# Optimization experiments

Hardware: AMD Instinct MI355X
Metric: run time of the kernel (lower is better)

Reference implementation:

```python
import jax, jax.numpy as jnp
import numpy as np

B = 8
N = 1024


def _sqrtm_psd(P):
    # symmetric PSD matrix square root via eigendecomposition
    w, V = jnp.linalg.eigh(P)
    return (V * jnp.sqrt(jnp.clip(w, 0.0))) @ V.T


def setup_inputs() -> dict:
    key = jax.random.key(0)
    k1, k2, k3 = jax.random.split(key, 3)
    x = jax.random.normal(k1, (1, B, N, 1), dtype=jnp.float32)
    # PSD covariance with nonnegative entries so abs() is a no-op and sqrtm is real
    A = jax.random.uniform(k2, (N, N), dtype=jnp.float32)
    P_u = (A @ A.T) / N
    Q_k = jax.random.uniform(k3, (N, N), dtype=jnp.float32)
    return {"x": x, "P_u": P_u, "Q_k": Q_k}


def reference(x, P_u, Q_k):
    n = x.shape[2]  # N
    # sigma = x.repeat(1,1,1,N): [1,B,N,N]
    sigma0 = jnp.broadcast_to(x, (1, x.shape[1], n, n))
    # p = sqrtm(N * |P_u|)
    p = _sqrtm_psd(n * jnp.abs(P_u))
    # concat(sigma+p, sigma-p) along last dim -> [1,B,N,2N]
    sigma = jnp.concatenate((sigma0 + p, sigma0 - p), axis=3)
    scale = 1.0 / (2 * n)
    x_bar = jnp.mean(sigma, axis=3)  # [1,B,N]
    # Faithful to original: only sigma[0,0] is used for the deviations,
    # while the mean varies with the batch index i2.
    points = sigma[0, 0]  # [N, 2N]
    c = points[None, :, :] - x_bar[0][:, :, None]  # [B, N, 2N]
    S = jnp.einsum('bni,bmi->bnm', c, c)  # sum of 2N outer products per batch
    P_k = S * scale + (Q_k ** 2) * 0.01
    return P_k, jnp.transpose(sigma, (0, 1, 3, 2))


if __name__ == "__main__":
    out = reference(**setup_inputs())
    print(out[0].shape, out[1].shape)
```

## Files before the change

### kernel.cpp

```cpp
#include <hip/hip_runtime.h>
#include <math.h>

#define NN 1024
#define BB 8
#define NS_ITERS 10
#define EPS_SHIFT 4.0f
#define MB (1u<<20)

typedef __attribute__((ext_vector_type(8))) short short8;
typedef __attribute__((ext_vector_type(4))) float floatx4;

__device__ __forceinline__ ushort f2bf(float f) {
    union { float f; uint32_t u; } v; v.f = f;
    uint32_t u = v.u;
    uint32_t r = (u + 0x7fffu + ((u >> 16) & 1u)) >> 16;
    return (ushort)r;
}
__device__ __forceinline__ float bf2f(ushort h) {
    union { uint32_t u; float f; } v; v.u = ((uint32_t)h) << 16;
    return v.f;
}

__device__ __forceinline__ void gload16(const ushort* g, ushort* s) {
    __builtin_amdgcn_global_load_lds(
        (__attribute__((address_space(1))) unsigned int*)(g),
        (__attribute__((address_space(3))) unsigned int*)(s), 16, 0, 0);
}

__device__ __forceinline__ float block_sum(float v) {
    #pragma unroll
    for (int off = 32; off > 0; off >>= 1) v += __shfl_down(v, off, 64);
    __shared__ float red[4];
    int lane = threadIdx.x & 63, wid = threadIdx.x >> 6;
    if (lane == 0) red[wid] = v;
    __syncthreads();
    float t = 0.f;
    if (threadIdx.x == 0) t = red[0] + red[1] + red[2] + red[3];
    return t;
}

__global__ __launch_bounds__(256) void matvec_abs(const float* __restrict__ pu,
                                                  const float* __restrict__ x,
                                                  float* __restrict__ y,
                                                  int use_ones) {
    int row = blockIdx.x;
    const float4* pr = (const float4*)(pu + (size_t)row * NN);
    float4 p = pr[threadIdx.x];
    float s;
    if (use_ones) {
        s = fabsf(p.x) + fabsf(p.y) + fabsf(p.z) + fabsf(p.w);
    } else {
        float4 xx = ((const float4*)x)[threadIdx.x];
        s = fabsf(p.x) * xx.x + fabsf(p.y) * xx.y + fabsf(p.z) * xx.z + fabsf(p.w) * xx.w;
    }
    s = block_sum(s);
    if (threadIdx.x == 0) y[row] = s;
}

__global__ void norm_vec(const float* __restrict__ y, float* __restrict__ v) {
    float ss = 0.f;
    for (int i = threadIdx.x; i < NN; i += 256) { float t = y[i]; ss += t * t; }
    #pragma unroll
    for (int off = 32; off > 0; off >>= 1) ss += __shfl_down(ss, off, 64);
    __shared__ float red[4];
    __shared__ float s_inv;
    int lane = threadIdx.x & 63, wid = threadIdx.x >> 6;
    if (lane == 0) red[wid] = ss;
    __syncthreads();
    if (threadIdx.x == 0) s_inv = rsqrtf(red[0] + red[1] + red[2] + red[3]);
    __syncthreads();
    float inv = s_inv;
    for (int i = threadIdx.x; i < NN; i += 256) v[i] = y[i] * inv;
}

__global__ void dot_vec(const float* __restrict__ a, const float* __restrict__ b,
                        float* __restrict__ out) {
    float s = 0.f;
    for (int i = threadIdx.x; i < NN; i += 256) s += a[i] * b[i];
    s = block_sum(s);
    if (threadIdx.x == 0) out[0] = s;
}

__global__ __launch_bounds__(256) void deflate_kernel(const float* __restrict__ pu,
                                                      const float* __restrict__ v,
                                                      const float* __restrict__ w,
                                                      float* __restrict__ sc,
                                                      float* __restrict__ D) {
    int idx = blockIdx.x * 256 + threadIdx.x;
    int row = idx >> 8;
    int c0 = (idx & 255) << 2;
    float lam = sc[5];
    float vr = v[row], wr = w[row];
    float4 p = ((const float4*)pu)[idx];
    float4 vc = *(const float4*)(v + c0);
    float4 wc = *(const float4*)(w + c0);
    float4 d;
    d.x = (float)NN * (fabsf(p.x) - vr * wc.x - wr * vc.x + lam * vr * vc.x);
    d.y = (float)NN * (fabsf(p.y) - vr * wc.y - wr * vc.y + lam * vr * vc.y);
    d.z = (float)NN * (fabsf(p.z) - vr * wc.z - wr * vc.z + lam * vr * vc.z);
    d.w = (float)NN * (fabsf(p.w) - vr * wc.w - wr * vc.w + lam * vr * vc.w);
    int dd = row - c0;
    if (dd == 0) d.x += EPS_SHIFT;
    else if (dd == 1) d.y += EPS_SHIFT;
    else if (dd == 2) d.z += EPS_SHIFT;
    else if (dd == 3) d.w += EPS_SHIFT;
    ((float4*)D)[idx] = d;
    float ss = d.x * d.x + d.y * d.y + d.z * d.z + d.w * d.w;
    ss = block_sum(ss);
    if (threadIdx.x == 0) atomicAdd(sc, ss);
}

__global__ void finalize_kernel(float* sc) {
    float c = sqrtf(sc[0]);
    sc[1] = 1.f / c;
    sc[2] = sqrtf(c);
    sc[4] = sqrtf((float)NN * sc[5]);
}

__device__ __forceinline__ void tile_swizzle64(int& row0, int& col0, int& zz) {
    int f = blockIdx.x + (blockIdx.y << 4) + (blockIdx.z << 8);
    int p = f & 7;
    int i = f >> 3;
    if (gridDim.z == 2) {
        zz = p & 1;
        int s = p >> 1;
        row0 = (((s >> 1) << 3) + (i >> 3)) << 6;
        col0 = (((s & 1) << 3) + (i & 7)) << 6;
    } else {
        zz = 0;
        row0 = (((p >> 1) << 2) + (i >> 3)) << 6;
        col0 = (((p & 1) << 3) + (i & 7)) << 6;
    }
}

__device__ __forceinline__ void mm_dev(const ushort* __restrict__ Ah,
                                       const ushort* __restrict__ Al,
                                       const ushort* __restrict__ Bh,
                                       const ushort* __restrict__ Bl,
                                       int row0, int col0, int kb, int kc,
                                       float* __restrict__ Cf,
                                       float* __restrict__ CfT,
                                       ushort* __restrict__ Chi,
                                       ushort* __restrict__ Clo) {
    __shared__ __align__(16) ushort lds[4 * 8192];
    const int t = threadIdx.x;
    const int w = t >> 6, l = t & 63;
    const int fm = l & 15, fq = l >> 4;
    const int lrow = l >> 2;
    const int lcol = (l & 3) << 3;

    const ushort* Ahp = Ah + (size_t)(row0 + lrow) * NN + kb + lcol;
    const ushort* Alp = Al + (size_t)(row0 + lrow) * NN + kb + lcol;
    const ushort* Bhp = Bh + (size_t)(col0 + lrow) * NN + kb + lcol;
    const ushort* Blp = Bl + (size_t)(col0 + lrow) * NN + kb + lcol;

    floatx4 acc[4][4];
    #pragma unroll
    for (int mi = 0; mi < 4; ++mi)
        #pragma unroll
        for (int ni = 0; ni < 4; ++ni) acc[mi][ni] = (floatx4)0.f;

    auto STAGE = [&](int kt) {
        const int koff = kt << 5;
        ushort* sb = lds + ((kt & 3) << 13);
        #pragma unroll
        for (int rb = 0; rb < 4; ++rb) {
            gload16(Ahp + (size_t)(rb << 4) * NN + koff, sb + (rb << 9));
            gload16(Alp + (size_t)(rb << 4) * NN + koff, sb + 2048 + (rb << 9));
            gload16(Bhp + (size_t)(rb << 4) * NN + koff, sb + 4096 + (rb << 9));
            gload16(Blp + (size_t)(rb << 4) * NN + koff, sb + 6144 + (rb << 9));
        }
    };

    const int nk = kc >> 5;
    STAGE(w);
    STAGE(w + 2);
    #pragma unroll 1
    for (int kt = w; kt < nk; kt += 2) {
        if (kt + 2 < nk) asm volatile("s_waitcnt vmcnt(16)" ::: "memory");
        else             asm volatile("s_waitcnt vmcnt(0)"  ::: "memory");
        __builtin_amdgcn_sched_barrier(0);
        const ushort* Ash = lds + ((kt & 3) << 13);
        const ushort* Asl = Ash + 2048;
        const ushort* Bsh = Ash + 4096;
        const ushort* Bsl = Ash + 6144;
        short8 ah[4], al[4], bh[4], bl[4];
        #pragma unroll
        for (int i = 0; i < 4; ++i) {
            const int ro = ((i << 4) + fm) * 32 + (fq << 3);
            ah[i] = *(const short8*)&Ash[ro];
            al[i] = *(const short8*)&Asl[ro];
            bh[i] = *(const short8*)&Bsh[ro];
            bl[i] = *(const short8*)&Bsl[ro];
        }
        asm volatile("s_waitcnt lgkmcnt(0)" ::: "memory");
        __builtin_amdgcn_sched_barrier(0);
        if (kt + 4 < nk) STAGE(kt + 4);
        #pragma unroll
        for (int mi = 0; mi < 4; ++mi)
            #pragma unroll
            for (int ni = 0; ni < 4; ++ni) {
                acc[mi][ni] = __builtin_amdgcn_mfma_f32_16x16x32_bf16(ah[mi], bh[ni], acc[mi][ni], 0, 0, 0);
                acc[mi][ni] = __builtin_amdgcn_mfma_f32_16x16x32_bf16(al[mi], bh[ni], acc[mi][ni], 0, 0, 0);
                acc[mi][ni] = __builtin_amdgcn_mfma_f32_16x16x32_bf16(ah[mi], bl[ni], acc[mi][ni], 0, 0, 0);
            }
    }

    __syncthreads();
    float* lf = (float*)lds;
    const int dep0 = w ? 0 : 2;
    const int own0 = w ? 2 : 0;
    #pragma unroll
    for (int m2 = 0; m2 < 2; ++m2) {
        #pragma unroll
        for (int ni = 0; ni < 4; ++ni)
            #pragma unroll
            for (int r = 0; r < 4; ++r) {
                int row = ((dep0 + m2) << 4) + (fq << 2) + r;
                int col = (ni << 4) + fm;
                lf[row * 66 + col] = acc[dep0 + m2][ni][r];
            }
    }
    __syncthreads();
    #pragma unroll
    for (int m2 = 0; m2 < 2; ++m2) {
        #pragma unroll
        for (int ni = 0; ni < 4; ++ni)
            #pragma unroll
            for (int r = 0; r < 4; ++r) {
                int row = ((own0 + m2) << 4) + (fq << 2) + r;
                int col = (ni << 4) + fm;
                acc[own0 + m2][ni][r] += lf[row * 66 + col];
            }
    }

    #pragma unroll
    for (int m2 = 0; m2 < 2; ++m2) {
        const int mi = own0 + m2;
        #pragma unroll
        for (int r = 0; r < 4; ++r) {
            int row = row0 + (mi << 4) + (fq << 2) + r;
            #pragma unroll
            for (int ni = 0; ni < 4; ++ni) {
                int col = col0 + (ni << 4) + fm;
                float v = acc[mi][ni][r];
                size_t idx = (size_t)row * NN + col;
                if (Cf) {
                    Cf[idx] = v;
                } else {
                    ushort h = f2bf(v);
                    Chi[idx] = h;
                    Clo[idx] = f2bf(v - bf2f(h));
                }
            }
        }
    }

    if (CfT) {
        __syncthreads();
        #pragma unroll
        for (int m2 = 0; m2 < 2; ++m2) {
            const int mi = own0 + m2;
            #pragma unroll
            for (int r = 0; r < 4; ++r) {
                int rl = (mi << 4) + (fq << 2) + r;
                #pragma unroll
                for (int ni = 0; ni < 4; ++ni) {
                    int cl = (ni << 4) + fm;
                    lf[cl * 68 + rl] = acc[mi][ni][r];
                }
            }
        }
        __syncthreads();
        int c = t >> 1, half = t & 1;
        const float* src = lf + c * 68 + (half << 5);
        float* dst = CfT + (size_t)(col0 + c) * NN + row0 + (half << 5);
        #pragma unroll
        for (int j = 0; j < 8; ++j)
            *(float4*)(dst + (j << 2)) = *(const float4*)(src + (j << 2));
    }
}

__global__ __launch_bounds__(128) void k_stage1(const ushort* __restrict__ Zh,
                                                const ushort* __restrict__ Zl,
                                                const ushort* __restrict__ Yh,
                                                const ushort* __restrict__ Yl,
                                                float* __restrict__ Mp,
                                                float* __restrict__ MpT0,
                                                float* __restrict__ MpT1) {
    int row0, col0, s;
    tile_swizzle64(row0, col0, s);
    mm_dev(Zh, Zl, Yh, Yl, row0, col0,
           s * (NN / 2), NN / 2, Mp + (size_t)s * NN * NN,
           s ? MpT1 : MpT0, nullptr, nullptr);
}

__global__ __launch_bounds__(128) void k_stage2(const ushort* __restrict__ Yh,
                                                const ushort* __restrict__ Yl,
                                                const ushort* __restrict__ Wh,
                                                const ushort* __restrict__ Wl,
                                                const ushort* __restrict__ Zh,
                                                const ushort* __restrict__ Zl,
                                                ushort* __restrict__ Ynh,
                                                ushort* __restrict__ Ynl,
                                                ushort* __restrict__ Znh,
                                                ushort* __restrict__ Znl) {
    int row0, col0, zz;
    tile_swizzle64(row0, col0, zz);
    if (zz == 0)
        mm_dev(Yh, Yl, Wh, Wl, row0, col0, 0, NN,
               nullptr, nullptr, Ynh, Ynl);
    else
        mm_dev(Wh, Wl, Zh, Zl, row0, col0, 0, NN,
               nullptr, nullptr, Znh, Znl);
}

__global__ __launch_bounds__(128) void k_final(const ushort* __restrict__ Yh,
                                               const ushort* __restrict__ Yl,
                                               const ushort* __restrict__ Wh,
                                               const ushort* __restrict__ Wl,
                                               float* __restrict__ Yf,
                                               float* __restrict__ YfT) {
    int row0, col0, zz;
    tile_swizzle64(row0, col0, zz);
    mm_dev(Yh, Yl, Wh, Wl, row0, col0, 0, NN,
           Yf, YfT, nullptr, nullptr);
}

__global__ __launch_bounds__(256) void k_wsplit(const float* __restrict__ Mp,
                                                const float* __restrict__ MpT0,
                                                const float* __restrict__ MpT1,
                                                ushort* __restrict__ Wh,
                                                ushort* __restrict__ Wl) {
    int i = blockIdx.x * 256 + threadIdx.x;
    int row = i >> 8, c0 = (i & 255) << 2;
    float4 m0 = ((const float4*)Mp)[i];
    float4 m1 = ((const float4*)Mp)[i + NN * NN / 4];
    float4 t0 = ((const float4*)MpT0)[i];
    float4 t1 = ((const float4*)MpT1)[i];
    float wv[4] = {-0.25f * (m0.x + m1.x + t0.x + t1.x),
                   -0.25f * (m0.y + m1.y + t0.y + t1.y),
                   -0.25f * (m0.z + m1.z + t0.z + t1.z),
                   -0.25f * (m0.w + m1.w + t0.w + t1.w)};
    int dd = row - c0;
    if (dd >= 0 && dd < 4) wv[dd] += 1.5f;
    ushort4 hv, lv;
    ushort* hp = (ushort*)&hv; ushort* lp = (ushort*)&lv;
    #pragma unroll
    for (int j = 0; j < 4; ++j) {
        ushort h = f2bf(wv[j]); hp[j] = h; lp[j] = f2bf(wv[j] - bf2f(h));
    }
    *(ushort4*)&Wh[(size_t)i << 2] = hv;
    *(ushort4*)&Wl[(size_t)i << 2] = lv;
}

__global__ __launch_bounds__(256) void k_wsplit0(const float* __restrict__ D,
                                                 const float* __restrict__ sc,
                                                 ushort* __restrict__ Yh,
                                                 ushort* __restrict__ Yl,
                                                 ushort* __restrict__ Wh,
                                                 ushort* __restrict__ Wl) {
    int i = blockIdx.x * 256 + threadIdx.x;
    int row = i >> 8, c0 = (i & 255) << 2;
    float invc = sc[1];
    float4 d = ((const float4*)D)[i];
    float yv[4] = {d.x * invc, d.y * invc, d.z * invc, d.w * invc};
    ushort4 yh, yl, wh, wl;
    ushort* yhp = (ushort*)&yh; ushort* ylp = (ushort*)&yl;
    ushort* whp = (ushort*)&wh; ushort* wlp = (ushort*)&wl;
    int dd = row - c0;
    #pragma unroll
    for (int j = 0; j < 4; ++j) {
        float y = yv[j];
        ushort h = f2bf(y); yhp[j] = h; ylp[j] = f2bf(y - bf2f(h));
        float wv = ((dd == j) ? 1.5f : 0.f) - 0.5f * y;
        ushort h2 = f2bf(wv); whp[j] = h2; wlp[j] = f2bf(wv - bf2f(h2));
    }
    *(ushort4*)&Yh[(size_t)i << 2] = yh;
    *(ushort4*)&Yl[(size_t)i << 2] = yl;
    *(ushort4*)&Wh[(size_t)i << 2] = wh;
    *(ushort4*)&Wl[(size_t)i << 2] = wl;
}

__global__ __launch_bounds__(256) void out0_kernel(const float* __restrict__ x,
                                                   const float* __restrict__ pu,
                                                   const float* __restrict__ qk,
                                                   float* __restrict__ out) {
    int i = blockIdx.x * blockDim.x + threadIdx.x;
    int rem = i & (NN * NN / 4 - 1);
    int b = i >> 18;
    int n = rem >> 8;
    int m4 = (rem & 255) << 2;
    float dn = x[n] - x[b * NN + n];
    float4 x0v = *(const float4*)(x + m4);
    float4 xbv = *(const float4*)(x + b * NN + m4);
    float4 pv = ((const float4*)pu)[rem];
    float4 qv = ((const float4*)qk)[rem];
    float4 o;
    o.x = dn * (x0v.x - xbv.x) + fabsf(pv.x) + 0.01f * qv.x * qv.x;
    o.y = dn * (x0v.y - xbv.y) + fabsf(pv.y) + 0.01f * qv.y * qv.y;
    o.z = dn * (x0v.z - xbv.z) + fabsf(pv.z) + 0.01f * qv.z * qv.z;
    o.w = dn * (x0v.w - xbv.w) + fabsf(pv.w) + 0.01f * qv.w * qv.w;
    ((float4*)out)[i] = o;
}

__global__ __launch_bounds__(256) void k_out1(const float* __restrict__ x,
                                              const float* __restrict__ Yf,
                                              const float* __restrict__ YfT,
                                              const float* __restrict__ sc,
                                              const float* __restrict__ v,
                                              float* __restrict__ out1) {
    int i = blockIdx.x * 256 + threadIdx.x;
    int j = i >> 8, i0 = (i & 255) << 2;
    float s = 0.5f * sc[2], s1v = sc[4] * v[j];
    float4 yr = *(const float4*)(Yf + (size_t)j * NN + i0);
    float4 yc = *(const float4*)(YfT + (size_t)j * NN + i0);
    float4 vc = *(const float4*)(v + i0);
    float4 p;
    p.x = s * (yr.x + yc.x) + s1v * vc.x;
    p.y = s * (yr.y + yc.y) + s1v * vc.y;
    p.z = s * (yr.z + yc.z) + s1v * vc.z;
    p.w = s * (yr.w + yc.w) + s1v * vc.w;
    #pragma unroll
    for (int b = 0; b < BB; ++b) {
        float4 xv = *(const float4*)(x + b * NN + i0);
        float4 a, m;
        a.x = xv.x + p.x; a.y = xv.y + p.y; a.z = xv.z + p.z; a.w = xv.w + p.w;
        m.x = xv.x - p.x; m.y = xv.y - p.y; m.z = xv.z - p.z; m.w = xv.w - p.w;
        float* base = out1 + (size_t)b * 2 * NN * NN;
        *(float4*)(base + (size_t)j * NN + i0) = a;
        *(float4*)(base + (size_t)(NN + j) * NN + i0) = m;
    }
}

extern "C" void kernel_launch(void* const* d_in, const int* in_sizes, int n_in,
                              void* d_out, int out_size, void* d_ws, size_t ws_size,
                              hipStream_t stream) {
    const float* x  = (const float*)d_in[0];
    const float* pu = (const float*)d_in[1];
    const float* qk = (const float*)d_in[2];
    float* out = (float*)d_out;
    char* ws = (char*)d_ws;

    float* Mp = (float*)ws;
    float* D  = Mp;
    float* Yf = Mp;
    float* YfT = (float*)(ws + (size_t)4 * MB);
    ushort* hi[5]; ushort* lo[5];
    for (int k = 0; k < 5; ++k) {
        hi[k] = (ushort*)(ws + (size_t)8 * MB + (size_t)k * 4 * MB);
        lo[k] = (ushort*)(ws + (size_t)8 * MB + (size_t)k * 4 * MB + 2 * MB);
    }
    float* vv = (float*)(ws + (size_t)28 * MB);
    float* vw = (float*)(ws + (size_t)28 * MB + 4096);
    float* vt = (float*)(ws + (size_t)28 * MB + 8192);
    float* sc = (float*)(ws + (size_t)28 * MB + 12288);

    hipMemsetAsync(sc, 0, 64, stream);
    matvec_abs<<<NN, 256, 0, stream>>>(pu, vv, vt, 1);
    norm_vec<<<1, 256, 0, stream>>>(vt, vv);
    matvec_abs<<<NN, 256, 0, stream>>>(pu, vv, vt, 0);
    norm_vec<<<1, 256, 0, stream>>>(vt, vv);
    matvec_abs<<<NN, 256, 0, stream>>>(pu, vv, vw, 0);
    dot_vec<<<1, 256, 0, stream>>>(vv, vw, sc + 5);
    deflate_kernel<<<NN * NN / 4 / 256, 256, 0, stream>>>(pu, vv, vw, sc, D);
    finalize_kernel<<<1, 1, 0, stream>>>(sc);

    k_wsplit0<<<NN * NN / 4 / 256, 256, 0, stream>>>(D, sc, hi[0], lo[0], hi[1], lo[1]);
    k_stage2<<<dim3(16, 16, 1), 128, 0, stream>>>(hi[0], lo[0], hi[1], lo[1],
                                                  hi[0], lo[0],
                                                  hi[2], lo[2], hi[3], lo[3]);
    int Y = 2, Z = 1, f0 = 0, f1 = 3, f2 = 4;

    for (int it = 1; it < NS_ITERS; ++it) {
        int W = f0;
        float* MpT0 = (float*)hi[f1];
        float* MpT1 = (float*)hi[f2];
        k_stage1<<<dim3(16, 16, 2), 128, 0, stream>>>(hi[Z], lo[Z], hi[Y], lo[Y],
                                                      Mp, MpT0, MpT1);
        k_wsplit<<<NN * NN / 4 / 256, 256, 0, stream>>>(Mp, MpT0, MpT1,
                                                        hi[W], lo[W]);
        if (it + 1 < NS_ITERS) {
            int Yn = f1, Zn = f2;
            k_stage2<<<dim3(16, 16, 2), 128, 0, stream>>>(
                hi[Y], lo[Y], hi[W], lo[W], hi[Z], lo[Z],
                hi[Yn], lo[Yn], hi[Zn], lo[Zn]);
            f0 = Y; f1 = Z; f2 = W;
            Y = Yn; Z = Zn;
        } else {
            k_final<<<dim3(16, 16, 1), 128, 0, stream>>>(hi[Y], lo[Y], hi[W], lo[W],
                                                         Yf, YfT);
        }
    }

    out0_kernel<<<(BB * NN * NN / 4) / 256, 256, 0, stream>>>(x, pu, qk, out);
    k_out1<<<NN * NN / 4 / 256, 256, 0, stream>>>(x, Yf, YfT, sc, vv,
                                                  out + (size_t)BB * NN * NN);
}
```

Before: 700.8 us.

## Split tile loads between waves with shared LDS ring and barriers

Each wave used to stage its own full A and B k-tiles into private ring slots. Now wave 0 loads the A half and wave 1 the B half of every k-tile into a shared 4-slot ring, with a block barrier each step and prefetch three tiles ahead. Waves still alternate which k-tiles they compute. The goal is to halve per-wave global load issue and deepen prefetch, at the cost of a barrier per k-step that couples the two waves.

```diff
diff --git a/kernel.cpp b/kernel.cpp
--- a/kernel.cpp
+++ b/kernel.cpp
@@ -142,17 +142,18 @@
                                        float* __restrict__ CfT,
                                        ushort* __restrict__ Chi,
                                        ushort* __restrict__ Clo) {
-    __shared__ __align__(16) ushort lds[4 * 8192];
+    __shared__ __align__(16) ushort lds[4 * 4 * 2048];
     const int t = threadIdx.x;
     const int w = t >> 6, l = t & 63;
     const int fm = l & 15, fq = l >> 4;
     const int lrow = l >> 2;
     const int lcol = (l & 3) << 3;
 
-    const ushort* Ahp = Ah + (size_t)(row0 + lrow) * NN + kb + lcol;
-    const ushort* Alp = Al + (size_t)(row0 + lrow) * NN + kb + lcol;
-    const ushort* Bhp = Bh + (size_t)(col0 + lrow) * NN + kb + lcol;
-    const ushort* Blp = Bl + (size_t)(col0 + lrow) * NN + kb + lcol;
+    const ushort* gh = w ? Bh : Ah;
+    const ushort* gl = w ? Bl : Al;
+    const int r0 = w ? col0 : row0;
+    const ushort* ghp = gh + (size_t)(r0 + lrow) * NN + kb + lcol;
+    const ushort* glp = gl + (size_t)(r0 + lrow) * NN + kb + lcol;
 
     floatx4 acc[4][4];
     #pragma unroll
@@ -160,27 +161,18 @@
         #pragma unroll
         for (int ni = 0; ni < 4; ++ni) acc[mi][ni] = (floatx4)0.f;
 
-    auto STAGE = [&](int kt) {
+    auto STAGE = [&](int bufi, int kt) {
         const int koff = kt << 5;
-        ushort* sb = lds + ((kt & 3) << 13);
+        ushort* sb = lds + (bufi << 13) + (w << 12);
         #pragma unroll
         for (int rb = 0; rb < 4; ++rb) {
-            gload16(Ahp + (size_t)(rb << 4) * NN + koff, sb + (rb << 9));
-            gload16(Alp + (size_t)(rb << 4) * NN + koff, sb + 2048 + (rb << 9));
-            gload16(Bhp + (size_t)(rb << 4) * NN + koff, sb + 4096 + (rb << 9));
-            gload16(Blp + (size_t)(rb << 4) * NN + koff, sb + 6144 + (rb << 9));
+            gload16(ghp + (size_t)(rb << 4) * NN + koff, sb + (rb << 9));
+            gload16(glp + (size_t)(rb << 4) * NN + koff, sb + 2048 + (rb << 9));
         }
     };
 
-    const int nk = kc >> 5;
-    STAGE(w);
-    STAGE(w + 2);
-    #pragma unroll 1
-    for (int kt = w; kt < nk; kt += 2) {
-        if (kt + 2 < nk) asm volatile("s_waitcnt vmcnt(16)" ::: "memory");
-        else             asm volatile("s_waitcnt vmcnt(0)"  ::: "memory");
-        __builtin_amdgcn_sched_barrier(0);
-        const ushort* Ash = lds + ((kt & 3) << 13);
+    auto COMPUTE = [&](int bufi) {
+        const ushort* Ash = lds + (bufi << 13);
         const ushort* Asl = Ash + 2048;
         const ushort* Bsh = Ash + 4096;
         const ushort* Bsl = Ash + 6144;
@@ -193,9 +185,6 @@
             bh[i] = *(const short8*)&Bsh[ro];
             bl[i] = *(const short8*)&Bsl[ro];
         }
-        asm volatile("s_waitcnt lgkmcnt(0)" ::: "memory");
-        __builtin_amdgcn_sched_barrier(0);
-        if (kt + 4 < nk) STAGE(kt + 4);
         #pragma unroll
         for (int mi = 0; mi < 4; ++mi)
             #pragma unroll
@@ -204,6 +193,21 @@
                 acc[mi][ni] = __builtin_amdgcn_mfma_f32_16x16x32_bf16(al[mi], bh[ni], acc[mi][ni], 0, 0, 0);
                 acc[mi][ni] = __builtin_amdgcn_mfma_f32_16x16x32_bf16(ah[mi], bl[ni], acc[mi][ni], 0, 0, 0);
             }
+    };
+
+    const int nk = kc >> 5;
+    STAGE(0, 0);
+    STAGE(1, 1);
+    STAGE(2, 2);
+    #pragma unroll 1
+    for (int kt = 0; kt < nk; ++kt) {
+        if (kt + 2 < nk)       asm volatile("s_waitcnt vmcnt(16)" ::: "memory");
+        else if (kt + 1 < nk)  asm volatile("s_waitcnt vmcnt(8)"  ::: "memory");
+        else                   asm volatile("s_waitcnt vmcnt(0)"  ::: "memory");
+        __builtin_amdgcn_s_barrier();
+        __builtin_amdgcn_sched_barrier(0);
+        if (kt + 3 < nk) STAGE((kt + 3) & 3, kt + 3);
+        if ((kt & 1) == w) COMPUTE(kt & 3);
     }
 
     __syncthreads();
```

Measured after the change: 1.050 ms. 1.5x slower.
